# Performance work log

Hardware: AMD Instinct MI355X
Metric: run time of the kernel (lower is better)

## Reference

```python
import jax, jax.numpy as jnp
import numpy as np

IN_CHS = 128
NUM_HEADS = 4
WIN = 7
N = WIN * WIN            # 49 tokens per window
QKDIM = 128              # ceil(in_chs/num_groups/num_heads)*num_heads
HEAD_DIM = QKDIM // NUM_HEADS
SCALE = HEAD_DIM ** -0.5
B = 4096                 # batch * num_windows


def _relative_position_index(win_h, win_w):
    coords = np.stack(np.meshgrid(np.arange(win_h), np.arange(win_w), indexing='ij'))  # [2,h,w]
    cf = coords.reshape(2, -1)                      # [2, N]
    rc = (cf[:, :, None] - cf[:, None, :]).transpose(1, 2, 0).astype(np.int64)  # [N,N,2]
    rc[:, :, 0] += win_h - 1
    rc[:, :, 1] += win_w - 1
    rc[:, :, 0] *= 2 * win_w - 1
    return rc.sum(-1)                               # [N, N]


def setup_inputs() -> dict:
    key = jax.random.key(0)
    ks = jax.random.split(key, 8)
    x = jax.random.normal(ks[0], (B, N, IN_CHS), dtype=jnp.float32)
    qk_w = jax.random.normal(ks[1], (2 * QKDIM, IN_CHS), dtype=jnp.float32) * 0.02
    qk_b = jnp.zeros((2 * QKDIM,), dtype=jnp.float32)
    v_w = jax.random.normal(ks[2], (IN_CHS, IN_CHS), dtype=jnp.float32) * 0.02
    v_b = jnp.zeros((IN_CHS,), dtype=jnp.float32)
    proj_w = jax.random.normal(ks[3], (IN_CHS, IN_CHS), dtype=jnp.float32) * 0.02
    proj_b = jnp.zeros((IN_CHS,), dtype=jnp.float32)
    bias_table = jax.random.normal(ks[4], ((2 * WIN - 1) * (2 * WIN - 1), NUM_HEADS), dtype=jnp.float32) * 0.02
    rel_idx = jnp.asarray(_relative_position_index(WIN, WIN))  # [N,N] int64
    return {"x": x, "qk_w": qk_w, "qk_b": qk_b, "v_w": v_w, "v_b": v_b,
            "proj_w": proj_w, "proj_b": proj_b, "bias_table": bias_table,
            "rel_idx": rel_idx}


def reference(x, qk_w, qk_b, v_w, v_b, proj_w, proj_b, bias_table, rel_idx):
    Bn, Nn, C = x.shape
    # fused q/k projection: [B,N,2*qkdim] -> q,k each [B,H,N,d]
    qk = (x @ qk_w.T + qk_b).reshape(Bn, Nn, 2, NUM_HEADS, HEAD_DIM)
    q = qk[:, :, 0].transpose(0, 2, 1, 3)
    k = qk[:, :, 1].transpose(0, 2, 1, 3)
    v = (x @ v_w.T + v_b).reshape(Bn, Nn, NUM_HEADS, -1).transpose(0, 2, 1, 3)
    # windowed QK^T with gathered relative-position bias
    attn = jnp.einsum('bhnd,bhmd->bhnm', q * SCALE, k)
    bias = bias_table[rel_idx.reshape(-1)].reshape(Nn, Nn, NUM_HEADS).transpose(2, 0, 1)
    attn = jax.nn.softmax(attn + bias[None], axis=-1)
    out = jnp.einsum('bhnm,bhmd->bhnd', attn, v).transpose(0, 2, 1, 3).reshape(Bn, Nn, -1)
    return out @ proj_w.T + proj_b
```

## Files before the change

kernel.cpp:

```cpp
#include <hip/hip_runtime.h>
#include <hip/hip_bf16.h>

typedef __attribute__((ext_vector_type(8))) __bf16 bf16x8;
typedef __attribute__((ext_vector_type(4))) short short4v;
typedef __attribute__((ext_vector_type(4))) float f32x4;

#define MFMA(a,b,c) __builtin_amdgcn_mfma_f32_16x16x32_bf16((a),(b),(c),0,0,0)
#define MFMA16(a,b,c) __builtin_amdgcn_mfma_f32_16x16x16bf16_1k((a),(b),(c),0,0,0)

#define XB 0u
#define QB 16384u
#define KB 32768u
#define VT 49152u

static __device__ __forceinline__ unsigned short f2u(float x) {
  return __builtin_bit_cast(unsigned short, static_cast<__bf16>(x));
}
static __device__ __forceinline__ unsigned long long pack4(float a, float b, float c, float d) {
  union { __bf16 h[4]; unsigned long long u; } z;
  z.h[0] = static_cast<__bf16>(a);
  z.h[1] = static_cast<__bf16>(b);
  z.h[2] = static_cast<__bf16>(c);
  z.h[3] = static_cast<__bf16>(d);
  return z.u;
}
static __device__ __forceinline__ unsigned long long pack4v(f32x4 v) {
  return pack4(v[0], v[1], v[2], v[3]);
}
static __device__ __forceinline__ short4v pack4s(float a, float b, float c, float d) {
  union { __bf16 h[4]; short4v s; } z;
  z.h[0] = static_cast<__bf16>(a);
  z.h[1] = static_cast<__bf16>(b);
  z.h[2] = static_cast<__bf16>(c);
  z.h[3] = static_cast<__bf16>(d);
  return z.s;
}
static __device__ __forceinline__ unsigned sw256(unsigned row, unsigned colb) {
  return (row << 8) + (colb ^ ((row & 7u) << 4));
}
static __device__ __forceinline__ unsigned sw128(unsigned row, unsigned colb) {
  return (row << 7) + (colb ^ ((row & 7u) << 4));
}

__global__ void rsa_prep(const float* __restrict__ qk_w, const float* __restrict__ v_w,
                         const float* __restrict__ proj_w, const float* __restrict__ bias_table,
                         unsigned short* __restrict__ wqk, unsigned short* __restrict__ wv,
                         unsigned short* __restrict__ wp, float* __restrict__ biasNN) {
  const float QSCALE = 0.17677669529663687f * 1.4426950408889634f;
  const float LOG2E = 1.4426950408889634f;
  int t = blockIdx.x * blockDim.x + threadIdx.x;
  int stride = gridDim.x * blockDim.x;
  for (int i = t; i < 256 * 128; i += stride) {
    float v = qk_w[i];
    if (i < 128 * 128) v *= QSCALE;
    wqk[i] = f2u(v);
  }
  for (int i = t; i < 128 * 128; i += stride) wv[i] = f2u(v_w[i]);
  for (int i = t; i < 128 * 128; i += stride) wp[i] = f2u(proj_w[i]);
  for (int i = t; i < 4 * 64 * 64; i += stride) {
    int h = i >> 12, r = (i >> 6) & 63, m = i & 63;
    float v = -1e9f;
    if (r < 49 && m < 49) {
      int ri = r / 7, rj = r - ri * 7, mi = m / 7, mj = m - mi * 7;
      int rel = (ri - mi + 6) * 13 + (rj - mj + 6);
      v = bias_table[rel * 4 + h];
    }
    biasNN[i] = v * LOG2E;
  }
}

__global__ __launch_bounds__(512, 4) void rsa_main(
    const float* __restrict__ x, const float* __restrict__ qk_bias,
    const float* __restrict__ v_bias, const float* __restrict__ proj_bias,
    const unsigned short* __restrict__ wqk, const unsigned short* __restrict__ wv,
    const unsigned short* __restrict__ wp, const float* __restrict__ biasNN,
    float* __restrict__ out) {
  __shared__ __align__(16) unsigned char LDS[65536];
  const int tid = threadIdx.x;
  const int w = tid >> 6;
  const int lane = tid & 63;
  const int c = lane & 15;
  const int g = lane >> 4;
  const int b = blockIdx.x;
  const float QBSCALE = 0.17677669529663687f * 1.4426950408889634f;

  {
    const f32x4* xp = reinterpret_cast<const f32x4*>(x + (size_t)b * 6272);
    for (int i = tid; i < 1568; i += 512) {
      f32x4 v = xp[i];
      unsigned row = (unsigned)i >> 5, c4 = (unsigned)i & 31u;
      *reinterpret_cast<unsigned long long*>(LDS + XB + sw256(row, c4 * 8)) = pack4v(v);
    }
    for (int i = tid; i < 480; i += 512) {
      unsigned row = 49 + ((unsigned)i >> 5), c4 = (unsigned)i & 31u;
      *reinterpret_cast<unsigned long long*>(LDS + XB + sw256(row, c4 * 8)) = 0ull;
    }
  }
  __syncthreads();

  __builtin_amdgcn_s_setprio(1);
#pragma unroll
  for (int mi = 0; mi < 2; ++mi) {
    const int mt = w + 8 * mi;
    bf16x8 a[4];
    const unsigned short* wrow = wqk + (mt * 16 + c) * 128 + g * 8;
#pragma unroll
    for (int ks = 0; ks < 4; ++ks) a[ks] = *reinterpret_cast<const bf16x8*>(wrow + ks * 32);
    f32x4 bias4 = *reinterpret_cast<const f32x4*>(qk_bias + mt * 16 + g * 4);
    if (mi == 0) { bias4[0] *= QBSCALE; bias4[1] *= QBSCALE; bias4[2] *= QBSCALE; bias4[3] *= QBSCALE; }
    f32x4 acc[4];
#pragma unroll
    for (int nt = 0; nt < 4; ++nt) acc[nt] = bias4;
#pragma unroll
    for (int ks = 0; ks < 4; ++ks) {
#pragma unroll
      for (int nt = 0; nt < 4; ++nt) {
        bf16x8 bf = *reinterpret_cast<const bf16x8*>(LDS + XB + sw256(nt * 16 + c, (ks * 32 + g * 8) * 2));
        acc[nt] = MFMA(a[ks], bf, acc[nt]);
      }
    }
    const unsigned base = (mi == 0) ? QB : KB;
    const unsigned colb = ((mt & 7) * 16 + g * 4) * 2;
#pragma unroll
    for (int nt = 0; nt < 4; ++nt)
      *reinterpret_cast<unsigned long long*>(LDS + base + sw256(nt * 16 + c, colb)) = pack4v(acc[nt]);
  }

  {
    const float vb = v_bias[w * 16 + c];
    bf16x8 bw[4];
    const unsigned short* wrow = wv + (w * 16 + c) * 128 + g * 8;
#pragma unroll
    for (int ks = 0; ks < 4; ++ks) bw[ks] = *reinterpret_cast<const bf16x8*>(wrow + ks * 32);
    f32x4 acc[4];
#pragma unroll
    for (int mt = 0; mt < 4; ++mt) acc[mt] = f32x4{vb, vb, vb, vb};
#pragma unroll
    for (int ks = 0; ks < 4; ++ks) {
#pragma unroll
      for (int mt = 0; mt < 4; ++mt) {
        bf16x8 af = *reinterpret_cast<const bf16x8*>(LDS + XB + sw256(mt * 16 + c, (ks * 32 + g * 8) * 2));
        acc[mt] = MFMA(af, bw[ks], acc[mt]);
      }
    }
#pragma unroll
    for (int mt = 0; mt < 4; ++mt)
      *reinterpret_cast<unsigned long long*>(LDS + VT + sw128(w * 16 + c, (mt * 16 + g * 4) * 2)) =
          pack4v(acc[mt]);
  }
  __builtin_amdgcn_s_setprio(0);
  __syncthreads();

  const int h = w >> 1;
  const int rt0 = (w & 1) * 2;

  f32x4 bb[2][4];
#pragma unroll
  for (int r2 = 0; r2 < 2; ++r2) {
    const float* bp = biasNN + ((h * 64 + (rt0 + r2) * 16 + c) << 6);
#pragma unroll
    for (int mt = 0; mt < 4; ++mt)
      bb[r2][mt] = *reinterpret_cast<const f32x4*>(bp + mt * 16 + g * 4);
  }

  f32x4 s[2][4];
  {
    bf16x8 kf[4];
#pragma unroll
    for (int mt = 0; mt < 4; ++mt)
      kf[mt] = *reinterpret_cast<const bf16x8*>(LDS + KB + sw256(mt * 16 + c, h * 64 + g * 16));
    __builtin_amdgcn_s_setprio(1);
#pragma unroll
    for (int r2 = 0; r2 < 2; ++r2) {
      bf16x8 qf = *reinterpret_cast<const bf16x8*>(LDS + QB + sw256((rt0 + r2) * 16 + c, h * 64 + g * 16));
#pragma unroll
      for (int mt = 0; mt < 4; ++mt)
        s[r2][mt] = MFMA(kf[mt], qf, bb[r2][mt]);
    }
    __builtin_amdgcn_s_setprio(0);
  }

  short4v pk[2][4];
#pragma unroll
  for (int r2 = 0; r2 < 2; ++r2) {
    float v[16];
#pragma unroll
    for (int mt = 0; mt < 4; ++mt) {
#pragma unroll
      for (int j = 0; j < 4; ++j) v[mt * 4 + j] = exp2f(s[r2][mt][j]);
    }
    float p0 = (v[0] + v[1]) + (v[2] + v[3]);
    float p1 = (v[4] + v[5]) + (v[6] + v[7]);
    float p2 = (v[8] + v[9]) + (v[10] + v[11]);
    float p3 = (v[12] + v[13]) + (v[14] + v[15]);
    float sum = (p0 + p1) + (p2 + p3);
    sum += __shfl_xor(sum, 16);
    sum += __shfl_xor(sum, 32);
    const float inv = __builtin_amdgcn_rcpf(sum);
#pragma unroll
    for (int mt = 0; mt < 4; ++mt)
      pk[r2][mt] = pack4s(v[mt * 4] * inv, v[mt * 4 + 1] * inv,
                          v[mt * 4 + 2] * inv, v[mt * 4 + 3] * inv);
  }

  f32x4 od[2][2];
  {
    short4v vfrag[2][4];
#pragma unroll
    for (int ct2 = 0; ct2 < 2; ++ct2)
#pragma unroll
      for (int ks = 0; ks < 4; ++ks)
        vfrag[ct2][ks] = *reinterpret_cast<const short4v*>(
            LDS + VT + sw128((h * 2 + ct2) * 16 + c, (ks * 16 + g * 4) * 2));
#pragma unroll
    for (int ct2 = 0; ct2 < 2; ++ct2)
#pragma unroll
      for (int r2 = 0; r2 < 2; ++r2) od[ct2][r2] = f32x4{0.f, 0.f, 0.f, 0.f};
    __builtin_amdgcn_s_setprio(1);
#pragma unroll
    for (int ks = 0; ks < 4; ++ks)
#pragma unroll
      for (int ct2 = 0; ct2 < 2; ++ct2)
#pragma unroll
        for (int r2 = 0; r2 < 2; ++r2)
          od[ct2][r2] = MFMA16(vfrag[ct2][ks], pk[r2][ks], od[ct2][r2]);
    __builtin_amdgcn_s_setprio(0);
  }

  bf16x8 ap[4];
  {
    const unsigned short* wrow = wp + (w * 16 + c) * 128 + g * 8;
#pragma unroll
    for (int ks = 0; ks < 4; ++ks) ap[ks] = *reinterpret_cast<const bf16x8*>(wrow + ks * 32);
  }
  f32x4 pb4 = *reinterpret_cast<const f32x4*>(proj_bias + w * 16 + g * 4);

#pragma unroll
  for (int ct2 = 0; ct2 < 2; ++ct2)
#pragma unroll
    for (int r2 = 0; r2 < 2; ++r2) {
      const int r = (rt0 + r2) * 16 + c;
      *reinterpret_cast<unsigned long long*>(
          LDS + XB + sw256(r, ((h * 2 + ct2) * 16 + g * 4) * 2)) = pack4v(od[ct2][r2]);
    }
  __syncthreads();

  {
    f32x4 acc[4];
#pragma unroll
    for (int nt = 0; nt < 4; ++nt) acc[nt] = pb4;
    __builtin_amdgcn_s_setprio(1);
#pragma unroll
    for (int ks = 0; ks < 4; ++ks) {
#pragma unroll
      for (int nt = 0; nt < 4; ++nt) {
        bf16x8 bf = *reinterpret_cast<const bf16x8*>(LDS + XB + sw256(nt * 16 + c, (ks * 32 + g * 8) * 2));
        acc[nt] = MFMA(ap[ks], bf, acc[nt]);
      }
    }
    __builtin_amdgcn_s_setprio(0);
#pragma unroll
    for (int nt = 0; nt < 4; ++nt) {
      const int tok = nt * 16 + c;
      if (tok < 49) {
        *reinterpret_cast<f32x4*>(out + ((size_t)b * 49 + tok) * 128 + w * 16 + g * 4) = acc[nt];
      }
    }
  }
}

extern "C" void kernel_launch(void* const* d_in, const int* in_sizes, int n_in,
                              void* d_out, int out_size, void* d_ws, size_t ws_size,
                              hipStream_t stream) {
  const float* x          = (const float*)d_in[0];
  const float* qk_w       = (const float*)d_in[1];
  const float* qk_b       = (const float*)d_in[2];
  const float* v_w        = (const float*)d_in[3];
  const float* v_b        = (const float*)d_in[4];
  const float* proj_w     = (const float*)d_in[5];
  const float* proj_b     = (const float*)d_in[6];
  const float* bias_table = (const float*)d_in[7];
  float* out = (float*)d_out;

  unsigned short* wqk = (unsigned short*)d_ws;
  unsigned short* wv  = wqk + 256 * 128;
  unsigned short* wp  = wv + 128 * 128;
  float* biasNN = (float*)((char*)d_ws + 131072);

  const int B = in_sizes[0] / (49 * 128);

  rsa_prep<<<dim3(128), dim3(512), 0, stream>>>(qk_w, v_w, proj_w, bias_table, wqk, wv, wp, biasNN);
  rsa_main<<<dim3(B), dim3(512), 0, stream>>>(x, qk_b, v_b, proj_b, wqk, wv, wp, biasNN, out);
}
```

Measured before the change: 120.0 us.

## Make each head's wave pair compute its own Q/K/V to drop the barrier

```diff
diff --git a/kernel.cpp b/kernel.cpp
--- a/kernel.cpp
+++ b/kernel.cpp
@@ -12,6 +12,7 @@
 #define QB 16384u
 #define KB 32768u
 #define VT 49152u
+#define OB 65536u
 
 static __device__ __forceinline__ unsigned short f2u(float x) {
   return __builtin_bit_cast(unsigned short, static_cast<__bf16>(x));
@@ -75,13 +76,16 @@
     const unsigned short* __restrict__ wqk, const unsigned short* __restrict__ wv,
     const unsigned short* __restrict__ wp, const float* __restrict__ biasNN,
     float* __restrict__ out) {
-  __shared__ __align__(16) unsigned char LDS[65536];
+  __shared__ __align__(16) unsigned char LDS[81920];
   const int tid = threadIdx.x;
   const int w = tid >> 6;
   const int lane = tid & 63;
   const int c = lane & 15;
   const int g = lane >> 4;
   const int b = blockIdx.x;
+  const int h = w >> 1;
+  const int half = w & 1;
+  const int rt0 = half * 2;
   const float QBSCALE = 0.17677669529663687f * 1.4426950408889634f;
 
   {
@@ -100,59 +104,72 @@
 
   __builtin_amdgcn_s_setprio(1);
 #pragma unroll
-  for (int mi = 0; mi < 2; ++mi) {
-    const int mt = w + 8 * mi;
+  for (int qi = 0; qi < 2; ++qi) {
+    const int qt = 2 * h + qi;
     bf16x8 a[4];
-    const unsigned short* wrow = wqk + (mt * 16 + c) * 128 + g * 8;
+    const unsigned short* wrow = wqk + (qt * 16 + c) * 128 + g * 8;
 #pragma unroll
     for (int ks = 0; ks < 4; ++ks) a[ks] = *reinterpret_cast<const bf16x8*>(wrow + ks * 32);
-    f32x4 bias4 = *reinterpret_cast<const f32x4*>(qk_bias + mt * 16 + g * 4);
-    if (mi == 0) { bias4[0] *= QBSCALE; bias4[1] *= QBSCALE; bias4[2] *= QBSCALE; bias4[3] *= QBSCALE; }
-    f32x4 acc[4];
-#pragma unroll
-    for (int nt = 0; nt < 4; ++nt) acc[nt] = bias4;
+    f32x4 bias4 = *reinterpret_cast<const f32x4*>(qk_bias + qt * 16 + g * 4);
+    bias4[0] *= QBSCALE; bias4[1] *= QBSCALE; bias4[2] *= QBSCALE; bias4[3] *= QBSCALE;
+#pragma unroll
+    for (int n2 = 0; n2 < 2; ++n2) {
+      const int nt = rt0 + n2;
+      f32x4 acc = bias4;
+#pragma unroll
+      for (int ks = 0; ks < 4; ++ks) {
+        bf16x8 bf = *reinterpret_cast<const bf16x8*>(LDS + XB + sw256(nt * 16 + c, (ks * 32 + g * 8) * 2));
+        acc = MFMA(a[ks], bf, acc);
+      }
+      *reinterpret_cast<unsigned long long*>(
+          LDS + QB + sw256(nt * 16 + c, (qt * 16 + g * 4) * 2)) = pack4v(acc);
+    }
+  }
+
+  {
+    f32x4 kacc[2][4], vacc[2][4];
+    {
+      f32x4 kb0 = *reinterpret_cast<const f32x4*>(qk_bias + 128 + (2 * h) * 16 + g * 4);
+      f32x4 kb1 = *reinterpret_cast<const f32x4*>(qk_bias + 128 + (2 * h + 1) * 16 + g * 4);
+      const float vb0 = v_bias[(2 * h) * 16 + c];
+      const float vb1 = v_bias[(2 * h + 1) * 16 + c];
+#pragma unroll
+      for (int nt = 0; nt < 4; ++nt) {
+        kacc[0][nt] = kb0;
+        kacc[1][nt] = kb1;
+        vacc[0][nt] = f32x4{vb0, vb0, vb0, vb0};
+        vacc[1][nt] = f32x4{vb1, vb1, vb1, vb1};
+      }
+    }
 #pragma unroll
     for (int ks = 0; ks < 4; ++ks) {
+      bf16x8 kw0 = *reinterpret_cast<const bf16x8*>(wqk + (128 + (2 * h) * 16 + c) * 128 + ks * 32 + g * 8);
+      bf16x8 kw1 = *reinterpret_cast<const bf16x8*>(wqk + (128 + (2 * h + 1) * 16 + c) * 128 + ks * 32 + g * 8);
+      bf16x8 vw0 = *reinterpret_cast<const bf16x8*>(wv + ((2 * h) * 16 + c) * 128 + ks * 32 + g * 8);
+      bf16x8 vw1 = *reinterpret_cast<const bf16x8*>(wv + ((2 * h + 1) * 16 + c) * 128 + ks * 32 + g * 8);
 #pragma unroll
       for (int nt = 0; nt < 4; ++nt) {
-        bf16x8 bf = *reinterpret_cast<const bf16x8*>(LDS + XB + sw256(nt * 16 + c, (ks * 32 + g * 8) * 2));
-        acc[nt] = MFMA(a[ks], bf, acc[nt]);
-      }
-    }
-    const unsigned base = (mi == 0) ? QB : KB;
-    const unsigned colb = ((mt & 7) * 16 + g * 4) * 2;
-#pragma unroll
-    for (int nt = 0; nt < 4; ++nt)
-      *reinterpret_cast<unsigned long long*>(LDS + base + sw256(nt * 16 + c, colb)) = pack4v(acc[nt]);
-  }
-
-  {
-    const float vb = v_bias[w * 16 + c];
-    bf16x8 bw[4];
-    const unsigned short* wrow = wv + (w * 16 + c) * 128 + g * 8;
-#pragma unroll
-    for (int ks = 0; ks < 4; ++ks) bw[ks] = *reinterpret_cast<const bf16x8*>(wrow + ks * 32);
-    f32x4 acc[4];
-#pragma unroll
-    for (int mt = 0; mt < 4; ++mt) acc[mt] = f32x4{vb, vb, vb, vb};
-#pragma unroll
-    for (int ks = 0; ks < 4; ++ks) {
-#pragma unroll
-      for (int mt = 0; mt < 4; ++mt) {
-        bf16x8 af = *reinterpret_cast<const bf16x8*>(LDS + XB + sw256(mt * 16 + c, (ks * 32 + g * 8) * 2));
-        acc[mt] = MFMA(af, bw[ks], acc[mt]);
-      }
-    }
-#pragma unroll
-    for (int mt = 0; mt < 4; ++mt)
-      *reinterpret_cast<unsigned long long*>(LDS + VT + sw128(w * 16 + c, (mt * 16 + g * 4) * 2)) =
-          pack4v(acc[mt]);
+        bf16x8 xf = *reinterpret_cast<const bf16x8*>(LDS + XB + sw256(nt * 16 + c, (ks * 32 + g * 8) * 2));
+        kacc[0][nt] = MFMA(kw0, xf, kacc[0][nt]);
+        kacc[1][nt] = MFMA(kw1, xf, kacc[1][nt]);
+        vacc[0][nt] = MFMA(xf, vw0, vacc[0][nt]);
+        vacc[1][nt] = MFMA(xf, vw1, vacc[1][nt]);
+      }
+    }
+#pragma unroll
+    for (int ki = 0; ki < 2; ++ki)
+#pragma unroll
+      for (int nt = 0; nt < 4; ++nt)
+        *reinterpret_cast<unsigned long long*>(
+            LDS + KB + sw256(nt * 16 + c, ((2 * h + ki) * 16 + g * 4) * 2)) = pack4v(kacc[ki][nt]);
+#pragma unroll
+    for (int ci = 0; ci < 2; ++ci)
+#pragma unroll
+      for (int nt = 0; nt < 4; ++nt)
+        *reinterpret_cast<unsigned long long*>(
+            LDS + VT + sw128((2 * h + ci) * 16 + c, (nt * 16 + g * 4) * 2)) = pack4v(vacc[ci][nt]);
   }
   __builtin_amdgcn_s_setprio(0);
-  __syncthreads();
-
-  const int h = w >> 1;
-  const int rt0 = (w & 1) * 2;
 
   f32x4 bb[2][4];
 #pragma unroll
@@ -241,7 +258,7 @@
     for (int r2 = 0; r2 < 2; ++r2) {
       const int r = (rt0 + r2) * 16 + c;
       *reinterpret_cast<unsigned long long*>(
-          LDS + XB + sw256(r, ((h * 2 + ct2) * 16 + g * 4) * 2)) = pack4v(od[ct2][r2]);
+          LDS + OB + sw256(r, ((h * 2 + ct2) * 16 + g * 4) * 2)) = pack4v(od[ct2][r2]);
     }
   __syncthreads();
 
@@ -254,7 +271,7 @@
     for (int ks = 0; ks < 4; ++ks) {
 #pragma unroll
       for (int nt = 0; nt < 4; ++nt) {
-        bf16x8 bf = *reinterpret_cast<const bf16x8*>(LDS + XB + sw256(nt * 16 + c, (ks * 32 + g * 8) * 2));
+        bf16x8 bf = *reinterpret_cast<const bf16x8*>(LDS + OB + sw256(nt * 16 + c, (ks * 32 + g * 8) * 2));
         acc[nt] = MFMA(ap[ks], bf, acc[nt]);
       }
     }
```

After: 155.7 us. 29.8% more time.

## Shrink LDS to 48KB by reusing X buffer for V and Q buffer for output

Applied to the files above, without the earlier changes.

```diff
diff --git a/kernel.cpp b/kernel.cpp
--- a/kernel.cpp
+++ b/kernel.cpp
@@ -11,7 +11,6 @@
 #define XB 0u
 #define QB 16384u
 #define KB 32768u
-#define VT 49152u
 
 static __device__ __forceinline__ unsigned short f2u(float x) {
   return __builtin_bit_cast(unsigned short, static_cast<__bf16>(x));
@@ -69,19 +68,21 @@
   }
 }
 
-__global__ __launch_bounds__(512, 4) void rsa_main(
+__global__ __launch_bounds__(512, 6) void rsa_main(
     const float* __restrict__ x, const float* __restrict__ qk_bias,
     const float* __restrict__ v_bias, const float* __restrict__ proj_bias,
     const unsigned short* __restrict__ wqk, const unsigned short* __restrict__ wv,
     const unsigned short* __restrict__ wp, const float* __restrict__ biasNN,
     float* __restrict__ out) {
-  __shared__ __align__(16) unsigned char LDS[65536];
+  __shared__ __align__(16) unsigned char LDS[49152];
   const int tid = threadIdx.x;
   const int w = tid >> 6;
   const int lane = tid & 63;
   const int c = lane & 15;
   const int g = lane >> 4;
   const int b = blockIdx.x;
+  const int h = w >> 1;
+  const int rt0 = (w & 1) * 2;
   const float QBSCALE = 0.17677669529663687f * 1.4426950408889634f;
 
   {
@@ -126,68 +127,56 @@
       *reinterpret_cast<unsigned long long*>(LDS + base + sw256(nt * 16 + c, colb)) = pack4v(acc[nt]);
   }
 
+  f32x4 vacc[4];
   {
     const float vb = v_bias[w * 16 + c];
     bf16x8 bw[4];
     const unsigned short* wrow = wv + (w * 16 + c) * 128 + g * 8;
 #pragma unroll
     for (int ks = 0; ks < 4; ++ks) bw[ks] = *reinterpret_cast<const bf16x8*>(wrow + ks * 32);
-    f32x4 acc[4];
-#pragma unroll
-    for (int mt = 0; mt < 4; ++mt) acc[mt] = f32x4{vb, vb, vb, vb};
+#pragma unroll
+    for (int mt = 0; mt < 4; ++mt) vacc[mt] = f32x4{vb, vb, vb, vb};
 #pragma unroll
     for (int ks = 0; ks < 4; ++ks) {
 #pragma unroll
       for (int mt = 0; mt < 4; ++mt) {
         bf16x8 af = *reinterpret_cast<const bf16x8*>(LDS + XB + sw256(mt * 16 + c, (ks * 32 + g * 8) * 2));
-        acc[mt] = MFMA(af, bw[ks], acc[mt]);
-      }
-    }
-#pragma unroll
-    for (int mt = 0; mt < 4; ++mt)
-      *reinterpret_cast<unsigned long long*>(LDS + VT + sw128(w * 16 + c, (mt * 16 + g * 4) * 2)) =
-          pack4v(acc[mt]);
+        vacc[mt] = MFMA(af, bw[ks], vacc[mt]);
+      }
+    }
   }
   __builtin_amdgcn_s_setprio(0);
   __syncthreads();
 
-  const int h = w >> 1;
-  const int rt0 = (w & 1) * 2;
-
-  f32x4 bb[2][4];
+#pragma unroll
+  for (int mt = 0; mt < 4; ++mt)
+    *reinterpret_cast<unsigned long long*>(LDS + XB + sw128(w * 16 + c, (mt * 16 + g * 4) * 2)) =
+        pack4v(vacc[mt]);
+
+  short4v pk[2][4];
 #pragma unroll
   for (int r2 = 0; r2 < 2; ++r2) {
-    const float* bp = biasNN + ((h * 64 + (rt0 + r2) * 16 + c) << 6);
-#pragma unroll
-    for (int mt = 0; mt < 4; ++mt)
-      bb[r2][mt] = *reinterpret_cast<const f32x4*>(bp + mt * 16 + g * 4);
-  }
-
-  f32x4 s[2][4];
-  {
-    bf16x8 kf[4];
-#pragma unroll
-    for (int mt = 0; mt < 4; ++mt)
-      kf[mt] = *reinterpret_cast<const bf16x8*>(LDS + KB + sw256(mt * 16 + c, h * 64 + g * 16));
+    f32x4 bbr[4];
+    {
+      const float* bp = biasNN + ((h * 64 + (rt0 + r2) * 16 + c) << 6);
+#pragma unroll
+      for (int mt = 0; mt < 4; ++mt)
+        bbr[mt] = *reinterpret_cast<const f32x4*>(bp + mt * 16 + g * 4);
+    }
+    bf16x8 qf = *reinterpret_cast<const bf16x8*>(LDS + QB + sw256((rt0 + r2) * 16 + c, h * 64 + g * 16));
+    f32x4 s[4];
     __builtin_amdgcn_s_setprio(1);
 #pragma unroll
-    for (int r2 = 0; r2 < 2; ++r2) {
-      bf16x8 qf = *reinterpret_cast<const bf16x8*>(LDS + QB + sw256((rt0 + r2) * 16 + c, h * 64 + g * 16));
-#pragma unroll
-      for (int mt = 0; mt < 4; ++mt)
-        s[r2][mt] = MFMA(kf[mt], qf, bb[r2][mt]);
+    for (int mt = 0; mt < 4; ++mt) {
+      bf16x8 kf = *reinterpret_cast<const bf16x8*>(LDS + KB + sw256(mt * 16 + c, h * 64 + g * 16));
+      s[mt] = MFMA(kf, qf, bbr[mt]);
     }
     __builtin_amdgcn_s_setprio(0);
-  }
-
-  short4v pk[2][4];
-#pragma unroll
-  for (int r2 = 0; r2 < 2; ++r2) {
     float v[16];
 #pragma unroll
     for (int mt = 0; mt < 4; ++mt) {
 #pragma unroll
-      for (int j = 0; j < 4; ++j) v[mt * 4 + j] = exp2f(s[r2][mt][j]);
+      for (int j = 0; j < 4; ++j) v[mt * 4 + j] = exp2f(s[mt][j]);
     }
     float p0 = (v[0] + v[1]) + (v[2] + v[3]);
     float p1 = (v[4] + v[5]) + (v[6] + v[7]);
@@ -202,6 +191,7 @@
       pk[r2][mt] = pack4s(v[mt * 4] * inv, v[mt * 4 + 1] * inv,
                           v[mt * 4 + 2] * inv, v[mt * 4 + 3] * inv);
   }
+  __syncthreads();
 
   f32x4 od[2][2];
   {
@@ -211,7 +201,7 @@
 #pragma unroll
       for (int ks = 0; ks < 4; ++ks)
         vfrag[ct2][ks] = *reinterpret_cast<const short4v*>(
-            LDS + VT + sw128((h * 2 + ct2) * 16 + c, (ks * 16 + g * 4) * 2));
+            LDS + XB + sw128((h * 2 + ct2) * 16 + c, (ks * 16 + g * 4) * 2));
 #pragma unroll
     for (int ct2 = 0; ct2 < 2; ++ct2)
 #pragma unroll
@@ -241,7 +231,7 @@
     for (int r2 = 0; r2 < 2; ++r2) {
       const int r = (rt0 + r2) * 16 + c;
       *reinterpret_cast<unsigned long long*>(
-          LDS + XB + sw256(r, ((h * 2 + ct2) * 16 + g * 4) * 2)) = pack4v(od[ct2][r2]);
+          LDS + QB + sw256(r, ((h * 2 + ct2) * 16 + g * 4) * 2)) = pack4v(od[ct2][r2]);
     }
   __syncthreads();
 
@@ -254,7 +244,7 @@
     for (int ks = 0; ks < 4; ++ks) {
 #pragma unroll
       for (int nt = 0; nt < 4; ++nt) {
-        bf16x8 bf = *reinterpret_cast<const bf16x8*>(LDS + XB + sw256(nt * 16 + c, (ks * 32 + g * 8) * 2));
+        bf16x8 bf = *reinterpret_cast<const bf16x8*>(LDS + QB + sw256(nt * 16 + c, (ks * 32 + g * 8) * 2));
         acc[nt] = MFMA(ap[ks], bf, acc[nt]);
       }
     }
```

Measured after the change: 120.2 us. About the same (+0.2%).
